# Kernel optimization log

Measured on AMD Instinct MI355X. Metric: run time of the kernel, lower is better.

Reference implementation:

```python
import jax, jax.numpy as jnp
import numpy as np

EMBED_DIM = 768
NUM_HEADS = 12
SEGMENT_LENGTHS = (2048, 4096, 8192)
DILATION_RATES = (1, 2, 4)
LN_EPS = 1e-5


def setup_inputs() -> dict:
    rng = jax.random.key(0)
    ks = jax.random.split(rng, 6)
    B, S, E = 2, 8192, EMBED_DIM
    xavier = (2.0 / (E + E)) ** 0.5  # xavier_normal std for square fan-in/out
    return {
        "query": jax.random.normal(ks[0], (B, S, E), jnp.float32),
        "key": jax.random.normal(ks[1], (B, S, E), jnp.float32),
        "value": jax.random.normal(ks[2], (B, S, E), jnp.float32),
        "qkv_w": jax.random.normal(ks[3], (3 * E, E), jnp.float32) * xavier,
        "qkv_b": jnp.zeros((3 * E,), jnp.float32),
        "ln_w": jnp.ones((E,), jnp.float32),
        "ln_b": jnp.zeros((E,), jnp.float32),
        "out_w": jax.random.normal(ks[4], (E, E), jnp.float32) * xavier,
        "out_b": jnp.zeros((E,), jnp.float32),
    }


def _dilated_attention(q, k, v):
    # q,k,v: [b, n, h, d].  Heads are partitioned across the
    # (segment_length, dilation_rate) groups; within each group the sequence
    # is split into segments of length s and subsampled with stride r at
    # offset (i % r); plain softmax attention runs inside each dilated segment.
    b, n, h, d = q.shape
    G = len(SEGMENT_LENGTHS)
    g = h // G
    scale = 1.0 / np.sqrt(d)
    out = jnp.zeros_like(q)
    for i, (s, r) in enumerate(zip(SEGMENT_LENGTHS, DILATION_RATES)):
        off = i % r
        h0, h1 = i * g, (i + 1) * g
        m = n // s
        def seg(x):
            # [b, n, g, d] -> [b, m, s/r, g, d]
            return x[:, :, h0:h1].reshape(b, m, s, g, d)[:, :, off::r]
        qi, ki, vi = seg(q), seg(k), seg(v)
        scores = jnp.einsum("bmqgd,bmkgd->bmgqk", qi, ki) * scale
        p = jax.nn.softmax(scores, axis=-1)
        xi = jnp.einsum("bmgqk,bmkgd->bmqgd", p, vi)
        seg_out = jnp.zeros((b, m, s, g, d), q.dtype).at[:, :, off::r].set(xi)
        out = out.at[:, :, h0:h1].set(seg_out.reshape(b, n, g, d))
    return out / G


def reference(query, key, value, qkv_w, qkv_b, ln_w, ln_b, out_w, out_b):
    B, S, E = query.shape
    H = NUM_HEADS
    d = E // H
    # fused QKV projection (cross-attention path of the fused projection)
    q = (query @ qkv_w[:E].T + qkv_b[:E]).reshape(B, S, H, d)
    k = (key @ qkv_w[E:2 * E].T + qkv_b[E:2 * E]).reshape(B, S, H, d)
    v = (value @ qkv_w[2 * E:].T + qkv_b[2 * E:]).reshape(B, S, H, d)
    x = _dilated_attention(q, k, v).reshape(B, S, E)
    # MAGNETO layer norm before output projection
    mu = jnp.mean(x, axis=-1, keepdims=True)
    var = jnp.mean(jnp.square(x - mu), axis=-1, keepdims=True)
    x = (x - mu) * jax.lax.rsqrt(var + LN_EPS) * ln_w + ln_b
    return x @ out_w.T + out_b
```

## Files before the change

kernel.cpp:

```cpp
#include <hip/hip_runtime.h>
#include <hip/hip_bf16.h>
#include <math.h>

typedef __bf16 bf16_t;
typedef __bf16 bf16x8 __attribute__((ext_vector_type(8)));
typedef float f32x4 __attribute__((ext_vector_type(4)));

__device__ __forceinline__ void async_ld16(const void* g, void* l) {
  __builtin_amdgcn_global_load_lds(
      (const __attribute__((address_space(1))) unsigned int*)g,
      (__attribute__((address_space(3))) unsigned int*)l, 16, 0, 0);
}

#define BATCH 2
#define SEQ   8192
#define EMB   768
#define NHEAD 12
#define HD    64
#define TOK   (BATCH*SEQ)
#define GATH_PER_B 57344

__device__ __forceinline__ int grp_off(int g) { return g == 0 ? 0 : (g == 1 ? 1 : 2); }
__device__ __forceinline__ int headoff(int h) {
  int g = h >> 2;
  int base = (g == 0) ? 0 : ((g == 1) ? 32768 : 49152);
  return base + (h & 3) * (8192 >> g);
}

__global__ void k_cast(const float* __restrict__ in, bf16_t* __restrict__ out, int n) {
  int i = (blockIdx.x * blockDim.x + threadIdx.x) * 4;
  if (i < n) {
    float4 v = *(const float4*)(in + i);
    bf16_t o[4] = {(bf16_t)v.x, (bf16_t)v.y, (bf16_t)v.z, (bf16_t)v.w};
    *(uint2*)(out + i) = *(uint2*)o;
  }
}

__global__ __launch_bounds__(256, 2)
void k_gemm_qkv(const bf16_t* __restrict__ qb, const bf16_t* __restrict__ kb,
                const bf16_t* __restrict__ vb, const bf16_t* __restrict__ wqkv,
                const float* __restrict__ qkv_bias,
                bf16_t* __restrict__ Qb, bf16_t* __restrict__ Kb, bf16_t* __restrict__ Vb) {
  const int N = 768, K = 768;
  int z = blockIdx.z;
  const bf16_t* A = (z == 0) ? qb : (z == 1) ? kb : vb;
  const bf16_t* W = wqkv + (size_t)z * N * K;
  const float* bias = qkv_bias + z * N;
  bf16_t* C = (z == 0) ? Qb : (z == 1) ? Kb : Vb;

  __shared__ bf16_t As[128][32];
  __shared__ bf16_t Bs[128][32];

  int tid = threadIdx.x;
  int wave = tid >> 6, lane = tid & 63;
  int q = lane >> 4, c = lane & 15;
  int wm = (wave & 1) * 64, wn = (wave >> 1) * 64;
  int m0 = blockIdx.y * 128, n0 = blockIdx.x * 128;

  f32x4 acc[4][4];
#pragma unroll
  for (int i = 0; i < 4; i++)
#pragma unroll
    for (int j = 0; j < 4; j++) acc[i][j] = (f32x4){0.f, 0.f, 0.f, 0.f};

  for (int k0 = 0; k0 < K; k0 += 32) {
#pragma unroll
    for (int it = 0; it < 2; ++it) {
      int ch = tid + it * 256;
      int row = ch >> 2, kb8 = (ch & 3) << 3;
      async_ld16(A + (size_t)(m0 + row) * K + k0 + kb8, &As[row][kb8]);
      async_ld16(W + (size_t)(n0 + row) * K + k0 + kb8, &Bs[row][kb8]);
    }
    __syncthreads();
    bf16x8 af[4], bfr[4];
#pragma unroll
    for (int mi = 0; mi < 4; mi++) af[mi] = *(const bf16x8*)&As[wm + mi * 16 + c][q * 8];
#pragma unroll
    for (int nj = 0; nj < 4; nj++) bfr[nj] = *(const bf16x8*)&Bs[wn + nj * 16 + c][q * 8];
#pragma unroll
    for (int mi = 0; mi < 4; mi++)
#pragma unroll
      for (int nj = 0; nj < 4; nj++)
        acc[mi][nj] = __builtin_amdgcn_mfma_f32_16x16x32_bf16(af[mi], bfr[nj], acc[mi][nj], 0, 0, 0);
    __syncthreads();
  }
  float qscale = (z == 0) ? 0.125f : 1.0f;
#pragma unroll
  for (int mi = 0; mi < 4; mi++)
#pragma unroll
    for (int nj = 0; nj < 4; nj++)
#pragma unroll
      for (int rg = 0; rg < 4; rg++) {
        int row = m0 + wm + mi * 16 + q * 4 + rg;
        int col = n0 + wn + nj * 16 + c;
        float v = (acc[mi][nj][rg] + bias[col]) * qscale;
        C[(size_t)row * N + col] = (bf16_t)v;
      }
}

__global__ __launch_bounds__(256, 2)
void k_gemm_out(const bf16_t* __restrict__ A, const bf16_t* __restrict__ W,
                const float* __restrict__ bias, float* __restrict__ C) {
  const int N = 768, K = 768;
  __shared__ bf16_t As[128][32];
  __shared__ bf16_t Bs[128][32];

  int tid = threadIdx.x;
  int wave = tid >> 6, lane = tid & 63;
  int q = lane >> 4, c = lane & 15;
  int wm = (wave & 1) * 64, wn = (wave >> 1) * 64;
  int m0 = blockIdx.y * 128, n0 = blockIdx.x * 128;

  f32x4 acc[4][4];
#pragma unroll
  for (int i = 0; i < 4; i++)
#pragma unroll
    for (int j = 0; j < 4; j++) acc[i][j] = (f32x4){0.f, 0.f, 0.f, 0.f};

  for (int k0 = 0; k0 < K; k0 += 32) {
#pragma unroll
    for (int it = 0; it < 2; ++it) {
      int ch = tid + it * 256;
      int row = ch >> 2, kb8 = (ch & 3) << 3;
      async_ld16(A + (size_t)(m0 + row) * K + k0 + kb8, &As[row][kb8]);
      async_ld16(W + (size_t)(n0 + row) * K + k0 + kb8, &Bs[row][kb8]);
    }
    __syncthreads();
    bf16x8 af[4], bfr[4];
#pragma unroll
    for (int mi = 0; mi < 4; mi++) af[mi] = *(const bf16x8*)&As[wm + mi * 16 + c][q * 8];
#pragma unroll
    for (int nj = 0; nj < 4; nj++) bfr[nj] = *(const bf16x8*)&Bs[wn + nj * 16 + c][q * 8];
#pragma unroll
    for (int mi = 0; mi < 4; mi++)
#pragma unroll
      for (int nj = 0; nj < 4; nj++)
        acc[mi][nj] = __builtin_amdgcn_mfma_f32_16x16x32_bf16(af[mi], bfr[nj], acc[mi][nj], 0, 0, 0);
    __syncthreads();
  }
#pragma unroll
  for (int mi = 0; mi < 4; mi++)
#pragma unroll
    for (int nj = 0; nj < 4; nj++)
#pragma unroll
      for (int rg = 0; rg < 4; rg++) {
        int row = m0 + wm + mi * 16 + q * 4 + rg;
        int col = n0 + wn + nj * 16 + c;
        C[(size_t)row * N + col] = acc[mi][nj][rg] + bias[col];
      }
}

__global__ __launch_bounds__(256)
void k_gather(const bf16_t* __restrict__ Qb, const bf16_t* __restrict__ Kb,
              const bf16_t* __restrict__ Vb,
              bf16_t* __restrict__ Qg, bf16_t* __restrict__ Kg, bf16_t* __restrict__ Vt) {
  int h = blockIdx.y, b = blockIdx.z;
  int g = h >> 2;
  int L = 8192 >> g;
  int jj0 = blockIdx.x * 128;
  if (jj0 >= L) return;
  int s = 2048 << g, off = grp_off(g);
  int hb = b * GATH_PER_B + headoff(h);
  int tid = threadIdx.x;

  __shared__ bf16_t tile[128][72];

#pragma unroll
  for (int it = 0; it < 4; ++it) {
    int ch = tid + it * 256;
    int rowl = ch >> 3, db = (ch & 7) << 3;
    int jj = jj0 + rowl;
    int p = (jj >> 11) * s + off + ((jj & 2047) << g);
    size_t src = ((size_t)(b * SEQ + p)) * EMB + h * HD + db;
    size_t dst = ((size_t)(hb + jj)) * HD + db;
    *(uint4*)(Qg + dst) = *(const uint4*)(Qb + src);
    *(uint4*)(Kg + dst) = *(const uint4*)(Kb + src);
    *(uint4*)&tile[rowl][db] = *(const uint4*)(Vb + src);
  }
  __syncthreads();
#pragma unroll
  for (int it = 0; it < 2; ++it) {
    int t2 = tid + it * 256;
    int dim = t2 >> 3, sg = t2 & 7;
    __attribute__((aligned(16))) bf16_t tmp[16];
#pragma unroll
    for (int jl = 0; jl < 16; jl++) {
      int j = ((jl & 7) << 4) + sg * 2 + (jl >> 3);
      tmp[jl] = tile[j][dim];
    }
    size_t vdst = ((size_t)hb) * HD + (size_t)dim * L + jj0 + sg * 16;
    *(uint4*)(Vt + vdst) = *(uint4*)&tmp[0];
    *(uint4*)(Vt + vdst + 8) = *(uint4*)&tmp[8];
  }
}

__global__ __launch_bounds__(256, 2)
void k_attn(const bf16_t* __restrict__ Qg, const bf16_t* __restrict__ Kg,
            const bf16_t* __restrict__ Vt, bf16_t* __restrict__ xattn) {
  int u = blockIdx.x;
  int seg = u % 56, qt = u / 56;
  int b = seg / 28, t = seg % 28;
  int g, h, si;
  if (t < 16)      { g = 0; h = t >> 2;              si = t & 3; }
  else if (t < 24) { g = 1; h = 4 + ((t - 16) >> 1); si = (t - 16) & 1; }
  else             { g = 2; h = 8 + (t - 24);        si = 0; }
  int L = 8192 >> g, s = 2048 << g, off = grp_off(g);
  int hb = b * GATH_PER_B + headoff(h);
  int jj0 = si * 2048 + qt * 128;
  int kvbase = si * 2048;

  __shared__ bf16_t Ps[128][128];
  __shared__ bf16_t Ks[128][64];
  __shared__ bf16_t Vs[64][128];

  int tid = threadIdx.x, wave = tid >> 6, lane = tid & 63;
  int q = lane >> 4, c = lane & 15;
  int cx = c & 7;
  int wm = wave * 32;

  bf16_t* Qs = &Ps[0][0];
#pragma unroll
  for (int it = 0; it < 4; ++it) {
    int ch = tid + it * 256;
    int row = ch >> 3, pc = ch & 7, lc = pc ^ (row & 7);
    async_ld16(Qg + ((size_t)(hb + jj0 + row)) * HD + lc * 8, Qs + ch * 8);
  }
  __syncthreads();
  bf16x8 aq[2][2];
#pragma unroll
  for (int mi = 0; mi < 2; mi++)
#pragma unroll
    for (int kq = 0; kq < 2; kq++) {
      int pch = (kq * 4 + q) ^ cx;
      aq[mi][kq] = *(const bf16x8*)(Qs + (size_t)(wm + mi * 16 + c) * HD + pch * 8);
    }

  float lrow[2][4];
  f32x4 O[2][4];
#pragma unroll
  for (int mi = 0; mi < 2; mi++)
#pragma unroll
    for (int rg = 0; rg < 4; rg++) lrow[mi][rg] = 0.f;
#pragma unroll
  for (int mi = 0; mi < 2; mi++)
#pragma unroll
    for (int vd = 0; vd < 4; vd++) O[mi][vd] = (f32x4){0.f, 0.f, 0.f, 0.f};

  for (int kt = 0; kt < 16; ++kt) {
    __syncthreads();
#pragma unroll
    for (int it = 0; it < 4; ++it) {
      int ch = tid + it * 256;
      int row = ch >> 3, pc = ch & 7, lc = pc ^ (row & 7);
      async_ld16(Kg + ((size_t)(hb + kvbase + kt * 128 + row)) * HD + lc * 8,
                 &Ks[0][0] + ch * 8);
    }
#pragma unroll
    for (int it = 0; it < 4; ++it) {
      int ch = tid + it * 256;
      int dim = ch >> 4, pc = ch & 15, lc = pc ^ (dim & 7);
      async_ld16(Vt + ((size_t)hb) * HD + (size_t)dim * L + kvbase + kt * 128 + lc * 8,
                 &Vs[0][0] + ch * 8);
    }
    __syncthreads();

    f32x4 Sv[2][8];
#pragma unroll
    for (int mi = 0; mi < 2; mi++)
#pragma unroll
      for (int nj = 0; nj < 8; nj++) Sv[mi][nj] = (f32x4){0.f, 0.f, 0.f, 0.f};
#pragma unroll
    for (int kq = 0; kq < 2; kq++) {
      int pch = (kq * 4 + q) ^ cx;
      bf16x8 bk[8];
#pragma unroll
      for (int nj = 0; nj < 8; nj++) bk[nj] = *(const bf16x8*)&Ks[nj * 16 + c][pch * 8];
#pragma unroll
      for (int mi = 0; mi < 2; mi++)
#pragma unroll
        for (int nj = 0; nj < 8; nj++)
          Sv[mi][nj] = __builtin_amdgcn_mfma_f32_16x16x32_bf16(aq[mi][kq], bk[nj], Sv[mi][nj], 0, 0, 0);
    }

#pragma unroll
    for (int mi = 0; mi < 2; mi++)
#pragma unroll
      for (int rg = 0; rg < 4; rg++) {
        bf16x8 p8;
        float rs = 0.f;
#pragma unroll
        for (int nj = 0; nj < 8; nj++) {
          float p = __expf(Sv[mi][nj][rg]);
          rs += p;
          p8[nj] = (bf16_t)p;
        }
        lrow[mi][rg] += rs;
        int row = wm + mi * 16 + q * 4 + rg;
        int pch = c ^ (row & 7);
        *(bf16x8*)&Ps[row][pch * 8] = p8;
      }

#pragma unroll
    for (int kk = 0; kk < 4; ++kk) {
      int pch = (kk * 4 + q) ^ cx;
      bf16x8 ap[2], bv[4];
#pragma unroll
      for (int mi = 0; mi < 2; mi++) ap[mi] = *(const bf16x8*)&Ps[wm + mi * 16 + c][pch * 8];
#pragma unroll
      for (int vd = 0; vd < 4; vd++) bv[vd] = *(const bf16x8*)&Vs[vd * 16 + c][pch * 8];
#pragma unroll
      for (int mi = 0; mi < 2; mi++)
#pragma unroll
        for (int vd = 0; vd < 4; vd++)
          O[mi][vd] = __builtin_amdgcn_mfma_f32_16x16x32_bf16(ap[mi], bv[vd], O[mi][vd], 0, 0, 0);
    }
  }

  const float inv3 = 1.0f / 3.0f;
#pragma unroll
  for (int mi = 0; mi < 2; mi++)
#pragma unroll
    for (int rg = 0; rg < 4; rg++) {
      float l = lrow[mi][rg];
#pragma unroll
      for (int d = 1; d < 16; d <<= 1) l += __shfl_xor(l, d, 64);
      float invl = inv3 / l;
      int jj = jj0 + wm + mi * 16 + q * 4 + rg;
      int p = si * s + off + ((jj & 2047) << g);
      size_t base = ((size_t)(b * SEQ + p)) * EMB + h * HD;
#pragma unroll
      for (int vd = 0; vd < 4; vd++)
        xattn[base + vd * 16 + c] = (bf16_t)(O[mi][vd][rg] * invl);
    }
}

__global__ __launch_bounds__(256)
void k_ln(const bf16_t* __restrict__ x, const float* __restrict__ lnw,
          const float* __restrict__ lnb, bf16_t* __restrict__ y) {
  int wave = threadIdx.x >> 6, lane = threadIdx.x & 63;
  int row = blockIdx.x * 4 + wave;
  const bf16_t* xr = x + (size_t)row * EMB;
  float v[12], s = 0.f, s2 = 0.f;
#pragma unroll
  for (int j = 0; j < 12; j++) {
    v[j] = (float)xr[lane + j * 64];
    s += v[j];
    s2 += v[j] * v[j];
  }
#pragma unroll
  for (int d = 1; d < 64; d <<= 1) { s += __shfl_xor(s, d, 64); s2 += __shfl_xor(s2, d, 64); }
  float mu = s * (1.f / 768.f);
  float var = s2 * (1.f / 768.f) - mu * mu;
  float rstd = rsqrtf(var + 1e-5f);
  bf16_t* yr = y + (size_t)row * EMB;
#pragma unroll
  for (int j = 0; j < 12; j++) {
    int e = lane + j * 64;
    yr[e] = (bf16_t)((v[j] - mu) * rstd * lnw[e] + lnb[e]);
  }
}

extern "C" void kernel_launch(void* const* d_in, const int* in_sizes, int n_in,
                              void* d_out, int out_size, void* d_ws, size_t ws_size,
                              hipStream_t stream) {
  const float* query = (const float*)d_in[0];
  const float* key   = (const float*)d_in[1];
  const float* value = (const float*)d_in[2];
  const float* qkv_w = (const float*)d_in[3];
  const float* qkv_b = (const float*)d_in[4];
  const float* ln_w  = (const float*)d_in[5];
  const float* ln_b  = (const float*)d_in[6];
  const float* out_w = (const float*)d_in[7];
  const float* out_b = (const float*)d_in[8];
  float* out = (float*)d_out;

  char* ws = (char*)d_ws;
  const size_t A = (size_t)TOK * EMB * 2;
  bf16_t* qb   = (bf16_t*)(ws + 0 * A);
  bf16_t* kb   = (bf16_t*)(ws + 1 * A);
  bf16_t* vb   = (bf16_t*)(ws + 2 * A);
  bf16_t* Qb   = (bf16_t*)(ws + 3 * A);
  bf16_t* Kb   = (bf16_t*)(ws + 4 * A);
  bf16_t* Vb   = (bf16_t*)(ws + 5 * A);
  bf16_t* wqkv = (bf16_t*)(ws + 6 * A);
  bf16_t* wout = (bf16_t*)(ws + 6 * A + (size_t)2304 * 768 * 2);
  bf16_t* Qg    = qb;
  bf16_t* Kg    = kb;
  bf16_t* Vt    = vb;
  bf16_t* xattn = Qb;
  bf16_t* xnorm = Kb;

  k_cast<<<12288, 256, 0, stream>>>(query, qb, TOK * EMB);
  k_cast<<<12288, 256, 0, stream>>>(key,   kb, TOK * EMB);
  k_cast<<<12288, 256, 0, stream>>>(value, vb, TOK * EMB);
  k_cast<<<1728, 256, 0, stream>>>(qkv_w, wqkv, 2304 * 768);
  k_cast<<<576, 256, 0, stream>>>(out_w, wout, 768 * 768);

  dim3 gq(6, 128, 3);
  k_gemm_qkv<<<gq, 256, 0, stream>>>(qb, kb, vb, wqkv, qkv_b, Qb, Kb, Vb);

  dim3 gg(64, 12, 2);
  k_gather<<<gg, 256, 0, stream>>>(Qb, Kb, Vb, Qg, Kg, Vt);

  hipMemsetAsync(xattn, 0, A, stream);
  k_attn<<<896, 256, 0, stream>>>(Qg, Kg, Vt, xattn);

  k_ln<<<4096, 256, 0, stream>>>(xattn, ln_w, ln_b, xnorm);

  dim3 go(6, 128);
  k_gemm_out<<<go, 256, 0, stream>>>(xnorm, wout, out_b, out);
}
```

Before: 453.5 us.

## Fuse input casts and Q/K gather into QKV GEMM, shrink attention LDS

Drops the three fp32-to-bf16 cast kernels for the activations: the QKV GEMM now reads fp32 inputs directly and converts them while staging into shared memory. The GEMM epilogue scatters Q and K rows straight into the dilated, gathered layout, skipping rows that no head group uses. The gather kernel then handles only the V transpose, with smaller 64-row tiles. Attention processes the P tile in two halves so the P buffer in LDS halves, and its launch bounds are raised to 3 blocks per CU. The cost is synchronous fp32 loads in the GEMM instead of async LDS loads, and scattered 2-byte stores in the epilogue.

Measured after the change: 465.9 us. +2.7%, slower.

```diff
diff --git a/kernel.cpp b/kernel.cpp
--- a/kernel.cpp
+++ b/kernel.cpp
@@ -4,6 +4,7 @@
 
 typedef __bf16 bf16_t;
 typedef __bf16 bf16x8 __attribute__((ext_vector_type(8)));
+typedef __bf16 bf16x4 __attribute__((ext_vector_type(4)));
 typedef float f32x4 __attribute__((ext_vector_type(4)));
 
 __device__ __forceinline__ void async_ld16(const void* g, void* l) {
@@ -20,7 +21,6 @@
 #define TOK   (BATCH*SEQ)
 #define GATH_PER_B 57344
 
-__device__ __forceinline__ int grp_off(int g) { return g == 0 ? 0 : (g == 1 ? 1 : 2); }
 __device__ __forceinline__ int headoff(int h) {
   int g = h >> 2;
   int base = (g == 0) ? 0 : ((g == 1) ? 32768 : 49152);
@@ -37,16 +37,15 @@
 }
 
 __global__ __launch_bounds__(256, 2)
-void k_gemm_qkv(const bf16_t* __restrict__ qb, const bf16_t* __restrict__ kb,
-                const bf16_t* __restrict__ vb, const bf16_t* __restrict__ wqkv,
+void k_gemm_qkv(const float* __restrict__ qf, const float* __restrict__ kf,
+                const float* __restrict__ vf, const bf16_t* __restrict__ wqkv,
                 const float* __restrict__ qkv_bias,
-                bf16_t* __restrict__ Qb, bf16_t* __restrict__ Kb, bf16_t* __restrict__ Vb) {
+                bf16_t* __restrict__ Qg, bf16_t* __restrict__ Kg, bf16_t* __restrict__ Vb) {
   const int N = 768, K = 768;
   int z = blockIdx.z;
-  const bf16_t* A = (z == 0) ? qb : (z == 1) ? kb : vb;
+  const float* A = (z == 0) ? qf : (z == 1) ? kf : vf;
   const bf16_t* W = wqkv + (size_t)z * N * K;
   const float* bias = qkv_bias + z * N;
-  bf16_t* C = (z == 0) ? Qb : (z == 1) ? Kb : Vb;
 
   __shared__ bf16_t As[128][32];
   __shared__ bf16_t Bs[128][32];
@@ -68,7 +67,13 @@
     for (int it = 0; it < 2; ++it) {
       int ch = tid + it * 256;
       int row = ch >> 2, kb8 = (ch & 3) << 3;
-      async_ld16(A + (size_t)(m0 + row) * K + k0 + kb8, &As[row][kb8]);
+      const float* src = A + (size_t)(m0 + row) * K + k0 + kb8;
+      float4 u0 = *(const float4*)src;
+      float4 u1 = *(const float4*)(src + 4);
+      __attribute__((aligned(16))) bf16_t t8[8] = {
+          (bf16_t)u0.x, (bf16_t)u0.y, (bf16_t)u0.z, (bf16_t)u0.w,
+          (bf16_t)u1.x, (bf16_t)u1.y, (bf16_t)u1.z, (bf16_t)u1.w};
+      *(uint4*)&As[row][kb8] = *(uint4*)t8;
       async_ld16(W + (size_t)(n0 + row) * K + k0 + kb8, &Bs[row][kb8]);
     }
     __syncthreads();
@@ -84,18 +89,43 @@
         acc[mi][nj] = __builtin_amdgcn_mfma_f32_16x16x32_bf16(af[mi], bfr[nj], acc[mi][nj], 0, 0, 0);
     __syncthreads();
   }
-  float qscale = (z == 0) ? 0.125f : 1.0f;
-#pragma unroll
-  for (int mi = 0; mi < 4; mi++)
-#pragma unroll
-    for (int nj = 0; nj < 4; nj++)
-#pragma unroll
-      for (int rg = 0; rg < 4; rg++) {
-        int row = m0 + wm + mi * 16 + q * 4 + rg;
-        int col = n0 + wn + nj * 16 + c;
-        float v = (acc[mi][nj][rg] + bias[col]) * qscale;
-        C[(size_t)row * N + col] = (bf16_t)v;
+
+  if (z == 2) {
+#pragma unroll
+    for (int mi = 0; mi < 4; mi++)
+#pragma unroll
+      for (int nj = 0; nj < 4; nj++)
+#pragma unroll
+        for (int rg = 0; rg < 4; rg++) {
+          int row = m0 + wm + mi * 16 + q * 4 + rg;
+          int col = n0 + wn + nj * 16 + c;
+          Vb[(size_t)row * N + col] = (bf16_t)(acc[mi][nj][rg] + bias[col]);
+        }
+  } else {
+    bf16_t* dst = (z == 0) ? Qg : Kg;
+    float qscale = (z == 0) ? 0.125f : 1.0f;
+#pragma unroll
+    for (int mi = 0; mi < 4; mi++)
+#pragma unroll
+      for (int nj = 0; nj < 4; nj++) {
+        int e = n0 + wn + nj * 16 + c;
+        int h = e >> 6, dim = e & 63, g2 = h >> 2;
+        int rm1 = (1 << g2) - 1, sh = 11 + g2;
+        int smask = (2048 << g2) - 1;
+        int ho = headoff(h);
+#pragma unroll
+        for (int rg = 0; rg < 4; rg++) {
+          int row = m0 + wm + mi * 16 + q * 4 + rg;
+          float v = (acc[mi][nj][rg] + bias[e]) * qscale;
+          int bb = row >> 13, p = row & 8191;
+          int t = (p & smask) - g2;
+          if (t >= 0 && (t & rm1) == 0) {
+            int jj = (p >> sh) * 2048 + (t >> g2);
+            dst[(size_t)(bb * GATH_PER_B + ho + jj) * HD + dim] = (bf16_t)v;
+          }
+        }
       }
+  }
 }
 
 __global__ __launch_bounds__(256, 2)
@@ -151,50 +181,41 @@
 }
 
 __global__ __launch_bounds__(256)
-void k_gather(const bf16_t* __restrict__ Qb, const bf16_t* __restrict__ Kb,
-              const bf16_t* __restrict__ Vb,
-              bf16_t* __restrict__ Qg, bf16_t* __restrict__ Kg, bf16_t* __restrict__ Vt) {
+void k_gather_v(const bf16_t* __restrict__ Vb, bf16_t* __restrict__ Vt) {
   int h = blockIdx.y, b = blockIdx.z;
   int g = h >> 2;
   int L = 8192 >> g;
-  int jj0 = blockIdx.x * 128;
+  int jj0 = blockIdx.x * 64;
   if (jj0 >= L) return;
-  int s = 2048 << g, off = grp_off(g);
+  int s = 2048 << g;
   int hb = b * GATH_PER_B + headoff(h);
   int tid = threadIdx.x;
 
-  __shared__ bf16_t tile[128][72];
-
-#pragma unroll
-  for (int it = 0; it < 4; ++it) {
+  __shared__ bf16_t tile[64][72];
+
+#pragma unroll
+  for (int it = 0; it < 2; ++it) {
     int ch = tid + it * 256;
     int rowl = ch >> 3, db = (ch & 7) << 3;
     int jj = jj0 + rowl;
-    int p = (jj >> 11) * s + off + ((jj & 2047) << g);
-    size_t src = ((size_t)(b * SEQ + p)) * EMB + h * HD + db;
-    size_t dst = ((size_t)(hb + jj)) * HD + db;
-    *(uint4*)(Qg + dst) = *(const uint4*)(Qb + src);
-    *(uint4*)(Kg + dst) = *(const uint4*)(Kb + src);
-    *(uint4*)&tile[rowl][db] = *(const uint4*)(Vb + src);
+    int p = (jj >> 11) * s + g + ((jj & 2047) << g);
+    *(uint4*)&tile[rowl][db] = *(const uint4*)(Vb + ((size_t)(b * SEQ + p)) * EMB + h * HD + db);
   }
   __syncthreads();
-#pragma unroll
-  for (int it = 0; it < 2; ++it) {
-    int t2 = tid + it * 256;
-    int dim = t2 >> 3, sg = t2 & 7;
-    __attribute__((aligned(16))) bf16_t tmp[16];
-#pragma unroll
-    for (int jl = 0; jl < 16; jl++) {
-      int j = ((jl & 7) << 4) + sg * 2 + (jl >> 3);
-      tmp[jl] = tile[j][dim];
-    }
-    size_t vdst = ((size_t)hb) * HD + (size_t)dim * L + jj0 + sg * 16;
-    *(uint4*)(Vt + vdst) = *(uint4*)&tmp[0];
-    *(uint4*)(Vt + vdst + 8) = *(uint4*)&tmp[8];
-  }
-}
-
-__global__ __launch_bounds__(256, 2)
+  int dim = tid >> 2, sub = tid & 3;
+  __attribute__((aligned(16))) bf16_t tmp[16];
+#pragma unroll
+  for (int sl = 0; sl < 16; sl++) {
+    int t = sub * 16 + sl;
+    int pos = (t & 3) * 16 + (t >> 2);
+    tmp[sl] = tile[pos][dim];
+  }
+  size_t vdst = ((size_t)hb) * HD + (size_t)dim * L + jj0 + sub * 16;
+  *(uint4*)(Vt + vdst) = *(uint4*)&tmp[0];
+  *(uint4*)(Vt + vdst + 8) = *(uint4*)&tmp[8];
+}
+
+__global__ __launch_bounds__(256, 3)
 void k_attn(const bf16_t* __restrict__ Qg, const bf16_t* __restrict__ Kg,
             const bf16_t* __restrict__ Vt, bf16_t* __restrict__ xattn) {
   int u = blockIdx.x;
@@ -204,12 +225,12 @@
   if (t < 16)      { g = 0; h = t >> 2;              si = t & 3; }
   else if (t < 24) { g = 1; h = 4 + ((t - 16) >> 1); si = (t - 16) & 1; }
   else             { g = 2; h = 8 + (t - 24);        si = 0; }
-  int L = 8192 >> g, s = 2048 << g, off = grp_off(g);
+  int L = 8192 >> g, s = 2048 << g;
   int hb = b * GATH_PER_B + headoff(h);
   int jj0 = si * 2048 + qt * 128;
   int kvbase = si * 2048;
 
-  __shared__ bf16_t Ps[128][128];
+  __shared__ bf16_t Ps[128][64];
   __shared__ bf16_t Ks[128][64];
   __shared__ bf16_t Vs[64][128];
 
@@ -283,36 +304,43 @@
     }
 
 #pragma unroll
-    for (int mi = 0; mi < 2; mi++)
-#pragma unroll
-      for (int rg = 0; rg < 4; rg++) {
-        bf16x8 p8;
-        float rs = 0.f;
-#pragma unroll
-        for (int nj = 0; nj < 8; nj++) {
-          float p = __expf(Sv[mi][nj][rg]);
-          rs += p;
-          p8[nj] = (bf16_t)p;
+    for (int half = 0; half < 2; ++half) {
+#pragma unroll
+      for (int mi = 0; mi < 2; mi++)
+#pragma unroll
+        for (int rg = 0; rg < 4; rg++) {
+          bf16x4 p4;
+          float rs = 0.f;
+#pragma unroll
+          for (int j = 0; j < 4; j++) {
+            float p = __expf(Sv[mi][half * 4 + j][rg]);
+            rs += p;
+            p4[j] = (bf16_t)p;
+          }
+          lrow[mi][rg] += rs;
+          int row = wm + mi * 16 + q * 4 + rg;
+          int u8 = c ^ ((row & 7) << 1);
+          *(bf16x4*)((char*)&Ps[row][0] + u8 * 8) = p4;
         }
-        lrow[mi][rg] += rs;
-        int row = wm + mi * 16 + q * 4 + rg;
-        int pch = c ^ (row & 7);
-        *(bf16x8*)&Ps[row][pch * 8] = p8;
+#pragma unroll
+      for (int kk2 = 0; kk2 < 2; ++kk2) {
+        bf16x8 ap[2], bv[4];
+#pragma unroll
+        for (int mi = 0; mi < 2; mi++) {
+          int u8 = (kk2 * 8 + q * 2) ^ (cx << 1);
+          ap[mi] = *(const bf16x8*)((char*)&Ps[wm + mi * 16 + c][0] + u8 * 8);
+        }
+#pragma unroll
+        for (int vd = 0; vd < 4; vd++) {
+          int pch = (half * 8 + kk2 * 4 + q) ^ cx;
+          bv[vd] = *(const bf16x8*)&Vs[vd * 16 + c][pch * 8];
+        }
+#pragma unroll
+        for (int mi = 0; mi < 2; mi++)
+#pragma unroll
+          for (int vd = 0; vd < 4; vd++)
+            O[mi][vd] = __builtin_amdgcn_mfma_f32_16x16x32_bf16(ap[mi], bv[vd], O[mi][vd], 0, 0, 0);
       }
-
-#pragma unroll
-    for (int kk = 0; kk < 4; ++kk) {
-      int pch = (kk * 4 + q) ^ cx;
-      bf16x8 ap[2], bv[4];
-#pragma unroll
-      for (int mi = 0; mi < 2; mi++) ap[mi] = *(const bf16x8*)&Ps[wm + mi * 16 + c][pch * 8];
-#pragma unroll
-      for (int vd = 0; vd < 4; vd++) bv[vd] = *(const bf16x8*)&Vs[vd * 16 + c][pch * 8];
-#pragma unroll
-      for (int mi = 0; mi < 2; mi++)
-#pragma unroll
-        for (int vd = 0; vd < 4; vd++)
-          O[mi][vd] = __builtin_amdgcn_mfma_f32_16x16x32_bf16(ap[mi], bv[vd], O[mi][vd], 0, 0, 0);
     }
   }
 
@@ -326,7 +354,7 @@
       for (int d = 1; d < 16; d <<= 1) l += __shfl_xor(l, d, 64);
       float invl = inv3 / l;
       int jj = jj0 + wm + mi * 16 + q * 4 + rg;
-      int p = si * s + off + ((jj & 2047) << g);
+      int p = si * s + g + ((jj & 2047) << g);
       size_t base = ((size_t)(b * SEQ + p)) * EMB + h * HD;
 #pragma unroll
       for (int vd = 0; vd < 4; vd++)
@@ -376,31 +404,23 @@
 
   char* ws = (char*)d_ws;
   const size_t A = (size_t)TOK * EMB * 2;
-  bf16_t* qb   = (bf16_t*)(ws + 0 * A);
-  bf16_t* kb   = (bf16_t*)(ws + 1 * A);
-  bf16_t* vb   = (bf16_t*)(ws + 2 * A);
-  bf16_t* Qb   = (bf16_t*)(ws + 3 * A);
-  bf16_t* Kb   = (bf16_t*)(ws + 4 * A);
-  bf16_t* Vb   = (bf16_t*)(ws + 5 * A);
-  bf16_t* wqkv = (bf16_t*)(ws + 6 * A);
-  bf16_t* wout = (bf16_t*)(ws + 6 * A + (size_t)2304 * 768 * 2);
-  bf16_t* Qg    = qb;
-  bf16_t* Kg    = kb;
-  bf16_t* Vt    = vb;
-  bf16_t* xattn = Qb;
-  bf16_t* xnorm = Kb;
-
-  k_cast<<<12288, 256, 0, stream>>>(query, qb, TOK * EMB);
-  k_cast<<<12288, 256, 0, stream>>>(key,   kb, TOK * EMB);
-  k_cast<<<12288, 256, 0, stream>>>(value, vb, TOK * EMB);
+  bf16_t* Qg    = (bf16_t*)(ws + 0 * A);
+  bf16_t* Kg    = (bf16_t*)(ws + 1 * A);
+  bf16_t* Vb    = (bf16_t*)(ws + 2 * A);
+  bf16_t* Vt    = (bf16_t*)(ws + 3 * A);
+  bf16_t* xattn = (bf16_t*)(ws + 4 * A);
+  bf16_t* xnorm = (bf16_t*)(ws + 5 * A);
+  bf16_t* wqkv  = (bf16_t*)(ws + 6 * A);
+  bf16_t* wout  = (bf16_t*)(ws + 6 * A + (size_t)2304 * 768 * 2);
+
   k_cast<<<1728, 256, 0, stream>>>(qkv_w, wqkv, 2304 * 768);
   k_cast<<<576, 256, 0, stream>>>(out_w, wout, 768 * 768);
 
   dim3 gq(6, 128, 3);
-  k_gemm_qkv<<<gq, 256, 0, stream>>>(qb, kb, vb, wqkv, qkv_b, Qb, Kb, Vb);
-
-  dim3 gg(64, 12, 2);
-  k_gather<<<gg, 256, 0, stream>>>(Qb, Kb, Vb, Qg, Kg, Vt);
+  k_gemm_qkv<<<gq, 256, 0, stream>>>(query, key, value, wqkv, qkv_b, Qg, Kg, Vb);
+
+  dim3 gg(128, 12, 2);
+  k_gather_v<<<gg, 256, 0, stream>>>(Vb, Vt);
 
   hipMemsetAsync(xattn, 0, A, stream);
   k_attn<<<896, 256, 0, stream>>>(Qg, Kg, Vt, xattn);
```
